# Kernel optimization log

Measured on AMD Instinct MI355X. Metric: run time of the kernel, lower is better.

The kernel has to match this reference:

```python
import jax, jax.numpy as jnp
import numpy as np

TEMP = 0.07
BASE_TEMP = 0.07
EPS = 1e-8


def setup_inputs() -> dict:
    key = jax.random.key(0)
    features = jax.random.normal(key, (4096, 2, 128), dtype=jnp.float32)
    return {"features": features}


def reference(features):
    B, V, D = features.shape  # bsz, n_views, dim
    # torch.cat(torch.unbind(features, dim=1), dim=0): view-major ordering
    cf = jnp.swapaxes(features, 0, 1).reshape(V * B, D)  # [N, D], N = V*B
    # cosine similarity = normalize rows then GEMM (same math as broadcasted CosineSimilarity)
    n = cf / jnp.maximum(jnp.linalg.norm(cf, axis=-1, keepdims=True), EPS)
    logits = jnp.matmul(n, n.T) / TEMP  # [N, N]
    N = V * B
    logits_mask = 1.0 - jnp.eye(N, dtype=logits.dtype)  # zero out self-contrast
    # SimCLR mask: eye(B) tiled over (anchor_count, contrast_count), minus diagonal
    pos_mask = jnp.tile(jnp.eye(B, dtype=logits.dtype), (V, V)) * logits_mask
    exp_logits = jnp.exp(logits) * logits_mask
    log_prob = logits - jnp.log(exp_logits.sum(axis=1, keepdims=True))
    mean_log_prob_pos = (pos_mask * log_prob).sum(axis=1) / pos_mask.sum(axis=1)
    loss = -(TEMP / BASE_TEMP) * mean_log_prob_pos
    return loss.reshape(V, B).mean()
```

## Files before the change

kernel.cpp:

```cpp
#include <hip/hip_runtime.h>
#include <hip/hip_bf16.h>
#include <math.h>


constexpr int   Bsz   = 4096;
constexpr int   Nrows = 8192;
constexpr int   Dd    = 128;
constexpr float TEMPf = 0.07f;
constexpr float EPSN  = 1e-8f;
constexpr float SCALE = 1.4426950408889634f / 0.07f;
constexpr float LN2   = 0.6931471805599453f;

constexpr int CHUNKS     = 16;
constexpr int CHUNK_COLS = Nrows / CHUNKS;
constexpr int TILE_COLS  = 64;
constexpr int TILES      = CHUNK_COLS / TILE_COLS;
constexpr int YGROUPS    = Nrows / 256;
constexpr int PREPBLKS   = Bsz / 4;
constexpr int TILE_BYTES = TILE_COLS * 256;

typedef __attribute__((ext_vector_type(8)))  short bf16x8;
typedef __attribute__((ext_vector_type(16))) float floatx16;

constexpr size_t OFF_NA   = 0x200000;
constexpr size_t OFF_PART = 0x400000;
constexpr size_t OFF_SPOS = 0x480000;

__global__ void prep_k(const float* __restrict__ f,
                       __hip_bfloat16* __restrict__ nB,
                       __hip_bfloat16* __restrict__ nA,
                       float* __restrict__ sposPart) {
    __shared__ float sred[4];
    int tid  = threadIdx.x;
    int wid  = tid >> 6;
    int lane = tid & 63;
    int b    = blockIdx.x * 4 + wid;

    const float* s0 = f + (size_t)(b * 2) * Dd;
    float2 x = *(const float2*)(s0 + lane * 2);
    float2 y = *(const float2*)(s0 + Dd + lane * 2);
    float ss0 = x.x * x.x + x.y * x.y;
    float ss1 = y.x * y.x + y.y * y.y;
    float dt  = x.x * y.x + x.y * y.y;
    #pragma unroll
    for (int off = 32; off; off >>= 1) {
        ss0 += __shfl_xor(ss0, off);
        ss1 += __shfl_xor(ss1, off);
        dt  += __shfl_xor(dt,  off);
    }
    float inv0 = 1.0f / fmaxf(sqrtf(ss0), EPSN);
    float inv1 = 1.0f / fmaxf(sqrtf(ss1), EPSN);
    __hip_bfloat162 h;
    h.x = __float2bfloat16(x.x * inv0);
    h.y = __float2bfloat16(x.y * inv0);
    *(__hip_bfloat162*)(nB + (size_t)b * Dd + lane * 2) = h;
    h.x = __float2bfloat16(x.x * inv0 * SCALE);
    h.y = __float2bfloat16(x.y * inv0 * SCALE);
    *(__hip_bfloat162*)(nA + (size_t)b * Dd + lane * 2) = h;
    h.x = __float2bfloat16(y.x * inv1);
    h.y = __float2bfloat16(y.y * inv1);
    *(__hip_bfloat162*)(nB + (size_t)(Bsz + b) * Dd + lane * 2) = h;
    h.x = __float2bfloat16(y.x * inv1 * SCALE);
    h.y = __float2bfloat16(y.y * inv1 * SCALE);
    *(__hip_bfloat162*)(nA + (size_t)(Bsz + b) * Dd + lane * 2) = h;

    if (lane == 0) sred[wid] = dt * inv0 * inv1 / TEMPf;
    __syncthreads();
    if (tid == 0) sposPart[blockIdx.x] = sred[0] + sred[1] + sred[2] + sred[3];
}

__global__ __launch_bounds__(256, 2)
void main_k(const __hip_bfloat16* __restrict__ nA, const __hip_bfloat16* __restrict__ nB,
            float* __restrict__ partial) {
    __shared__ char lds[2][TILE_BYTES];
    const int tid  = threadIdx.x;
    const int wid  = tid >> 6;
    const int lane = tid & 63;
    const int lo   = lane & 31;
    const int hi   = lane >> 5;
    const int rbase = blockIdx.y * 256 + wid * 64;
    const int cbase = blockIdx.x * CHUNK_COLS;
    const char* abytes = (const char*)nA;
    const char* gb     = (const char*)nB + (size_t)cbase * 256;
    const int su = tid & 15, scb = tid >> 4;

    uint4 pf[4];
    #pragma unroll
    for (int i = 0; i < 4; i++)
        pf[i] = *(const uint4*)(gb + i * 4096 + tid * 16);

    bf16x8 afrag[2][8];
    #pragma unroll
    for (int s = 0; s < 2; s++) {
        const char* rowp = abytes + (size_t)(rbase + s * 32 + lo) * 256 + hi * 16;
        #pragma unroll
        for (int kc = 0; kc < 8; kc++)
            afrag[s][kc] = *(const bf16x8*)(rowp + kc * 32);
    }

    #pragma unroll
    for (int i = 0; i < 4; i++) {
        int c = i * 16 + scb;
        *(uint4*)&lds[0][su * 1024 + ((c ^ su) & 63) * 16] = pf[i];
    }
    __syncthreads();

    float sums[2][16];
    #pragma unroll
    for (int s = 0; s < 2; s++)
        #pragma unroll
        for (int r = 0; r < 16; r++) sums[s][r] = 0.f;

    floatx16 zero = {};

    for (int t = 0; t < TILES; t++) {
        if (t + 1 < TILES) {
            const char* g = gb + (size_t)(t + 1) * TILE_BYTES;
            #pragma unroll
            for (int i = 0; i < 4; i++)
                pf[i] = *(const uint4*)(g + i * 4096 + tid * 16);
        }

        const char* buf = lds[t & 1];
        floatx16 acc[2][2];
        acc[0][0] = zero; acc[0][1] = zero; acc[1][0] = zero; acc[1][1] = zero;
        #pragma unroll
        for (int kc = 0; kc < 8; kc++) {
            int u = kc * 2 + hi;
            int a0 = u * 1024 + ((lo ^ u) & 63) * 16;
            bf16x8 b0 = *(const bf16x8*)&buf[a0];
            bf16x8 b1 = *(const bf16x8*)&buf[a0 ^ 512];
            acc[0][0] = __builtin_amdgcn_mfma_f32_32x32x16_bf16(afrag[0][kc], b0, acc[0][0], 0, 0, 0);
            acc[1][0] = __builtin_amdgcn_mfma_f32_32x32x16_bf16(afrag[1][kc], b0, acc[1][0], 0, 0, 0);
            acc[0][1] = __builtin_amdgcn_mfma_f32_32x32x16_bf16(afrag[0][kc], b1, acc[0][1], 0, 0, 0);
            acc[1][1] = __builtin_amdgcn_mfma_f32_32x32x16_bf16(afrag[1][kc], b1, acc[1][1], 0, 0, 0);
        }

        bool dtile = (cbase + t * TILE_COLS == rbase);
        #pragma unroll
        for (int s = 0; s < 2; s++)
            #pragma unroll
            for (int cg = 0; cg < 2; cg++) {
                #pragma unroll
                for (int r = 0; r < 16; r++) {
                    float e = __builtin_amdgcn_exp2f(acc[s][cg][r]);
                    if (dtile && cg == s && lo == ((r & 3) + 8 * (r >> 2) + 4 * hi))
                        e = 0.f;
                    sums[s][r] += e;
                }
            }

        if (t + 1 < TILES) {
            char* wb = lds[(t + 1) & 1];
            #pragma unroll
            for (int i = 0; i < 4; i++) {
                int c = i * 16 + scb;
                *(uint4*)&wb[su * 1024 + ((c ^ su) & 63) * 16] = pf[i];
            }
        }
        __syncthreads();
    }

    #pragma unroll
    for (int s = 0; s < 2; s++)
        #pragma unroll
        for (int r = 0; r < 16; r++) {
            float v = sums[s][r];
            #pragma unroll
            for (int off = 1; off < 32; off <<= 1) v += __shfl_xor(v, off);
            sums[s][r] = v;
        }
    if (lo == 0) {
        float* prow = partial + (size_t)blockIdx.x * Nrows;
        #pragma unroll
        for (int s = 0; s < 2; s++)
            #pragma unroll
            for (int r = 0; r < 16; r++) {
                int grow = rbase + s * 32 + (r & 3) + 8 * (r >> 2) + 4 * hi;
                prow[grow] = sums[s][r];
            }
    }
}

__global__ __launch_bounds__(1024)
void final_k(const float* __restrict__ partial, const float* __restrict__ sposPart,
             float* __restrict__ out) {
    __shared__ float red[16];
    int tid = threadIdx.x;
    float acc = 0.f;
    for (int r = tid; r < Nrows; r += 1024) {
        float se = 0.f;
        #pragma unroll
        for (int c = 0; c < CHUNKS; c++) se += partial[(size_t)c * Nrows + r];
        acc += __builtin_amdgcn_logf(se) * LN2;
    }
    for (int i = tid; i < PREPBLKS; i += 1024) acc -= 2.f * sposPart[i];
    #pragma unroll
    for (int off = 32; off; off >>= 1) acc += __shfl_xor(acc, off);
    if ((tid & 63) == 0) red[tid >> 6] = acc;
    __syncthreads();
    if (tid == 0) {
        float tt = 0.f;
        for (int w = 0; w < 16; w++) tt += red[w];
        out[0] = tt / (float)Nrows;
    }
}

extern "C" void kernel_launch(void* const* d_in, const int* in_sizes, int n_in,
                              void* d_out, int out_size, void* d_ws, size_t ws_size,
                              hipStream_t stream) {
    const float* f = (const float*)d_in[0];
    char* ws = (char*)d_ws;
    __hip_bfloat16* nB = (__hip_bfloat16*)ws;
    __hip_bfloat16* nA = (__hip_bfloat16*)(ws + OFF_NA);
    float* partial     = (float*)(ws + OFF_PART);
    float* sposPart    = (float*)(ws + OFF_SPOS);

    prep_k<<<PREPBLKS, 256, 0, stream>>>(f, nB, nA, sposPart);
    dim3 grid(CHUNKS, YGROUPS);
    main_k<<<grid, 256, 0, stream>>>(nA, nB, partial);
    final_k<<<1, 1024, 0, stream>>>(partial, sposPart, (float*)d_out);
}
```

Baseline: 87.69 us.

## Exploit Gram matrix symmetry: compute upper-triangle blocks with row and column sums

Because the similarity matrix is symmetric, the main kernel now computes only the upper-triangular 256x256 block pairs (528 blocks instead of 1024). Each off-diagonal block adds its exp values both to row sums and, via a cross-wave column reduction in LDS, to column sums for the mirrored rows. The final reduction is spread over 32 blocks that combine their results with an atomicAdd, and the output is zeroed in the prep kernel. This halves the MFMA and exp work. In exchange it adds column accumulators, an LDS reduction step, and a small serial loop that maps the block index to a tile pair. Summation order also differs, and the atomic combine is non-deterministic.

```diff
diff --git a/kernel.cpp b/kernel.cpp
--- a/kernel.cpp
+++ b/kernel.cpp
@@ -11,30 +11,30 @@
 constexpr float SCALE = 1.4426950408889634f / 0.07f;
 constexpr float LN2   = 0.6931471805599453f;
 
-constexpr int CHUNKS     = 16;
-constexpr int CHUNK_COLS = Nrows / CHUNKS;
+constexpr int G          = 32;
+constexpr int NBLK       = G * (G + 1) / 2;
 constexpr int TILE_COLS  = 64;
-constexpr int TILES      = CHUNK_COLS / TILE_COLS;
-constexpr int YGROUPS    = Nrows / 256;
+constexpr int TILE_BYTES = TILE_COLS * 256;
 constexpr int PREPBLKS   = Bsz / 4;
-constexpr int TILE_BYTES = TILE_COLS * 256;
 
 typedef __attribute__((ext_vector_type(8)))  short bf16x8;
 typedef __attribute__((ext_vector_type(16))) float floatx16;
 
 constexpr size_t OFF_NA   = 0x200000;
 constexpr size_t OFF_PART = 0x400000;
-constexpr size_t OFF_SPOS = 0x480000;
+constexpr size_t OFF_SPOS = 0x500000;
 
 __global__ void prep_k(const float* __restrict__ f,
                        __hip_bfloat16* __restrict__ nB,
                        __hip_bfloat16* __restrict__ nA,
-                       float* __restrict__ sposPart) {
+                       float* __restrict__ sposPart,
+                       float* __restrict__ out) {
     __shared__ float sred[4];
     int tid  = threadIdx.x;
     int wid  = tid >> 6;
     int lane = tid & 63;
     int b    = blockIdx.x * 4 + wid;
+    if (blockIdx.x == 0 && tid == 0) out[0] = 0.f;
 
     const float* s0 = f + (size_t)(b * 2) * Dd;
     float2 x = *(const float2*)(s0 + lane * 2);
@@ -78,10 +78,15 @@
     const int lane = tid & 63;
     const int lo   = lane & 31;
     const int hi   = lane >> 5;
-    const int rbase = blockIdx.y * 256 + wid * 64;
-    const int cbase = blockIdx.x * CHUNK_COLS;
+
+    int bb = blockIdx.x, gi = 0;
+    while (bb >= G - gi) { bb -= G - gi; gi++; }
+    const int gj = gi + bb;
+    const bool diag = (gi == gj);
+
+    const int rbase = gi * 256 + wid * 64;
     const char* abytes = (const char*)nA;
-    const char* gb     = (const char*)nB + (size_t)cbase * 256;
+    const char* gb = (const char*)nB + (size_t)gj * 256 * 256;
     const int su = tid & 15, scb = tid >> 4;
 
     uint4 pf[4];
@@ -110,11 +115,15 @@
     for (int s = 0; s < 2; s++)
         #pragma unroll
         for (int r = 0; r < 16; r++) sums[s][r] = 0.f;
+    float csum[4][2];
+    #pragma unroll
+    for (int t = 0; t < 4; t++) { csum[t][0] = 0.f; csum[t][1] = 0.f; }
 
     floatx16 zero = {};
 
-    for (int t = 0; t < TILES; t++) {
-        if (t + 1 < TILES) {
+    #pragma unroll
+    for (int t = 0; t < 4; t++) {
+        if (t < 3) {
             const char* g = gb + (size_t)(t + 1) * TILE_BYTES;
             #pragma unroll
             for (int i = 0; i < 4; i++)
@@ -136,7 +145,7 @@
             acc[1][1] = __builtin_amdgcn_mfma_f32_32x32x16_bf16(afrag[1][kc], b1, acc[1][1], 0, 0, 0);
         }
 
-        bool dtile = (cbase + t * TILE_COLS == rbase);
+        const bool dt_hit = diag && (t == wid);
         #pragma unroll
         for (int s = 0; s < 2; s++)
             #pragma unroll
@@ -144,13 +153,14 @@
                 #pragma unroll
                 for (int r = 0; r < 16; r++) {
                     float e = __builtin_amdgcn_exp2f(acc[s][cg][r]);
-                    if (dtile && cg == s && lo == ((r & 3) + 8 * (r >> 2) + 4 * hi))
+                    if (dt_hit && cg == s && lo == ((r & 3) + 8 * (r >> 2) + 4 * hi))
                         e = 0.f;
-                    sums[s][r] += e;
+                    sums[s][r]  += e;
+                    csum[t][cg] += e;
                 }
             }
 
-        if (t + 1 < TILES) {
+        if (t < 3) {
             char* wb = lds[(t + 1) & 1];
             #pragma unroll
             for (int i = 0; i < 4; i++) {
@@ -171,7 +181,7 @@
             sums[s][r] = v;
         }
     if (lo == 0) {
-        float* prow = partial + (size_t)blockIdx.x * Nrows;
+        float* prow = partial + (size_t)gj * Nrows;
         #pragma unroll
         for (int s = 0; s < 2; s++)
             #pragma unroll
@@ -180,30 +190,44 @@
                 prow[grow] = sums[s][r];
             }
     }
-}
-
-__global__ __launch_bounds__(1024)
+
+    if (!diag) {
+        float* colred = (float*)lds[0];
+        #pragma unroll
+        for (int t = 0; t < 4; t++)
+            #pragma unroll
+            for (int cg = 0; cg < 2; cg++)
+                csum[t][cg] += __shfl_xor(csum[t][cg], 32);
+        if (hi == 0) {
+            #pragma unroll
+            for (int t = 0; t < 4; t++)
+                #pragma unroll
+                for (int cg = 0; cg < 2; cg++)
+                    colred[wid * 256 + t * 64 + cg * 32 + lo] = csum[t][cg];
+        }
+        __syncthreads();
+        float v = colred[tid] + colred[256 + tid] + colred[512 + tid] + colred[768 + tid];
+        partial[(size_t)gi * Nrows + gj * 256 + tid] = v;
+    }
+}
+
+__global__ __launch_bounds__(256)
 void final_k(const float* __restrict__ partial, const float* __restrict__ sposPart,
              float* __restrict__ out) {
-    __shared__ float red[16];
-    int tid = threadIdx.x;
-    float acc = 0.f;
-    for (int r = tid; r < Nrows; r += 1024) {
-        float se = 0.f;
-        #pragma unroll
-        for (int c = 0; c < CHUNKS; c++) se += partial[(size_t)c * Nrows + r];
-        acc += __builtin_amdgcn_logf(se) * LN2;
-    }
-    for (int i = tid; i < PREPBLKS; i += 1024) acc -= 2.f * sposPart[i];
+    __shared__ float red[4];
+    int g = blockIdx.x, tid = threadIdx.x;
+    int r = g * 256 + tid;
+    float se = 0.f;
+    #pragma unroll
+    for (int p = 0; p < G; p++) se += partial[(size_t)p * Nrows + r];
+    float acc = __builtin_amdgcn_logf(se) * LN2;
+    if (tid < 32) acc -= 2.f * sposPart[g * 32 + tid];
     #pragma unroll
     for (int off = 32; off; off >>= 1) acc += __shfl_xor(acc, off);
     if ((tid & 63) == 0) red[tid >> 6] = acc;
     __syncthreads();
-    if (tid == 0) {
-        float tt = 0.f;
-        for (int w = 0; w < 16; w++) tt += red[w];
-        out[0] = tt / (float)Nrows;
-    }
+    if (tid == 0)
+        atomicAdd(out, (red[0] + red[1] + red[2] + red[3]) / (float)Nrows);
 }
 
 extern "C" void kernel_launch(void* const* d_in, const int* in_sizes, int n_in,
@@ -216,8 +240,7 @@
     float* partial     = (float*)(ws + OFF_PART);
     float* sposPart    = (float*)(ws + OFF_SPOS);
 
-    prep_k<<<PREPBLKS, 256, 0, stream>>>(f, nB, nA, sposPart);
-    dim3 grid(CHUNKS, YGROUPS);
-    main_k<<<grid, 256, 0, stream>>>(nA, nB, partial);
-    final_k<<<1, 1024, 0, stream>>>(partial, sposPart, (float*)d_out);
-}
+    prep_k<<<PREPBLKS, 256, 0, stream>>>(f, nB, nA, sposPart, (float*)d_out);
+    main_k<<<NBLK, 256, 0, stream>>>(nA, nB, partial);
+    final_k<<<G, 256, 0, stream>>>(partial, sposPart, (float*)d_out);
+}
```

Measured after the change: 138.7 us. 58.1% more time.
